# Performance work log

Measured on AMD Instinct MI355X. Metric: run time of the kernel, lower is better.

Reference implementation:

```python
import jax, jax.numpy as jnp
import numpy as np

ALPHA = 2.0
K_HOPS = 3
N_NODES, N_EDGES, IN_DIM = 8192, 131072, 128


def _mlp(coeffs, W0, W1, W2, W3):
    # MLP(n_layers=n_hidden_layers+2=4, relu between, no bias, bn/dropout off in eval)
    h = jax.nn.relu(coeffs @ W0)
    h = jax.nn.relu(h @ W1)
    h = jax.nn.relu(h @ W2)
    return h @ W3  # [N, 1] rotation angles


def _aggregate_k_hop(edge_index, angles):
    # Faithful translation of aggregate_k_hop including its in-place aliasing:
    # enhanced_angles aliases angles, and step_k ACCUMULATES across hops
    # (torch_scatter reduces into the provided out tensor).
    N = angles.shape[0]
    row, col = edge_index[0], edge_index[1]
    f = lambda k: jnp.exp(jnp.asarray(-ALPHA * k, angles.dtype))
    # hop 1: scatter-add over the raw edge list (duplicate edges counted, as in original)
    step = jax.ops.segment_sum(angles[col] * f(1), row, num_segments=N)
    enhanced = angles + step
    # Dense boolean adjacency: composing paths then np.unique(axis=1) is exactly the
    # 'exists a k-step walk' indicator, i.e. boolean adjacency powers.
    adj = jnp.zeros((N, N), jnp.float32).at[row, col].set(1.0)
    P = adj
    for k in range(2, K_HOPS + 1):
        P = ((P @ adj) > 0).astype(jnp.float32)  # unique k-walk pairs
        step = step + f(k) * (P @ enhanced)      # reads angles AFTER previous in-place add
        enhanced = enhanced + step               # step accumulates across hops
    return enhanced


def setup_inputs() -> dict:
    key = jax.random.key(0)
    k0, k1, k2, k3, k4, k5 = jax.random.split(key, 6)
    s = 1.0 / np.sqrt(IN_DIM)
    return {
        "coeffs": jax.random.normal(k0, (N_NODES, IN_DIM), jnp.float32),
        "W0": jax.random.normal(k1, (IN_DIM, IN_DIM), jnp.float32) * s,
        "W1": jax.random.normal(k2, (IN_DIM, IN_DIM), jnp.float32) * s,
        "W2": jax.random.normal(k3, (IN_DIM, IN_DIM), jnp.float32) * s,
        "W3": jax.random.normal(k4, (IN_DIM, 1), jnp.float32) * s,
        "edge_index": jax.random.randint(k5, (2, N_EDGES), 0, N_NODES, dtype=jnp.int32),
    }


def reference(coeffs, W0, W1, W2, W3, edge_index):
    angles = _mlp(coeffs, W0, W1, W2, W3)
    return _aggregate_k_hop(edge_index, angles)  # batch.node_rotation_angles, [N, 1]
```

## Files before the change

kernel.cpp:

```cpp
#include <hip/hip_runtime.h>

constexpr int N    = 8192;
constexpr int NE   = 131072;
constexpr int WPR  = N / 32;
constexpr int MAXD = 64;

#define F1 0.13533528323661270f
#define F2 0.018315638888734179f
#define F3 0.0024787521766663585f

using bf16x8 = __attribute__((ext_vector_type(8))) short;
using f32x4  = __attribute__((ext_vector_type(4))) float;

__device__ __forceinline__ unsigned short f2bf(float f) {
    unsigned int u = __float_as_uint(f);
    u = (u + 0x7FFFu + ((u >> 16) & 1u)) >> 16;
    return (unsigned short)u;
}

__global__ __launch_bounds__(256) void mlp_kernel(
    const float* __restrict__ X,
    const float* __restrict__ W0, const float* __restrict__ W1,
    const float* __restrict__ W2, const float* __restrict__ W3,
    float* __restrict__ angles, float* __restrict__ e1,
    uint4* __restrict__ cntz)
{
    __shared__ unsigned short Xb[16 * 136];
    __shared__ unsigned short Wt[128 * 136];
    __shared__ float part[4][16];

    const int tid  = threadIdx.x;
    const int row0 = blockIdx.x * 16;
    const int nh = tid >> 6, l = tid & 63;
    const int lm = l & 15, lq = l >> 4;

    if (tid < 4) {
        uint4 z; z.x = z.y = z.z = z.w = 0u;
        cntz[blockIdx.x * 4 + tid] = z;
    }

    for (int q = tid; q < 512; q += 256) {
        float4 v = *(const float4*)&X[row0 * 128 + q * 4];
        ushort4 b;
        b.x = f2bf(v.x); b.y = f2bf(v.y); b.z = f2bf(v.z); b.w = f2bf(v.w);
        *(ushort4*)&Xb[(q >> 5) * 136 + (q & 31) * 4] = b;
    }

    for (int layer = 0; layer < 3; ++layer) {
        const float* __restrict__ W = (layer == 0) ? W0 : (layer == 1) ? W1 : W2;
        for (int it = 0; it < 16; ++it) {
            int flat = it * 256 + tid;
            int n  = flat & 127;
            int k0 = (flat >> 7) << 2;
            ushort4 b;
            b.x = f2bf(W[(k0 + 0) * 128 + n]);
            b.y = f2bf(W[(k0 + 1) * 128 + n]);
            b.z = f2bf(W[(k0 + 2) * 128 + n]);
            b.w = f2bf(W[(k0 + 3) * 128 + n]);
            *(ushort4*)&Wt[n * 136 + k0] = b;
        }
        __syncthreads();

        f32x4 acc[2];
#pragma unroll
        for (int t = 0; t < 2; ++t) acc[t] = (f32x4){0.f, 0.f, 0.f, 0.f};

#pragma unroll
        for (int kc = 0; kc < 4; ++kc) {
            bf16x8 a = *(const bf16x8*)&Xb[lm * 136 + kc * 32 + lq * 8];
#pragma unroll
            for (int t = 0; t < 2; ++t) {
                bf16x8 b = *(const bf16x8*)
                    &Wt[(nh * 32 + t * 16 + lm) * 136 + kc * 32 + lq * 8];
                acc[t] = __builtin_amdgcn_mfma_f32_16x16x32_bf16(a, b, acc[t], 0, 0, 0);
            }
        }

#pragma unroll
        for (int t = 0; t < 2; ++t)
#pragma unroll
            for (int r = 0; r < 4; ++r) acc[t][r] = fmaxf(acc[t][r], 0.0f);

        __syncthreads();

        if (layer < 2) {
#pragma unroll
            for (int t = 0; t < 2; ++t)
#pragma unroll
                for (int r = 0; r < 4; ++r)
                    Xb[(lq * 4 + r) * 136 + nh * 32 + t * 16 + lm] =
                        f2bf(acc[t][r]);
        } else {
            float p[4] = {0.f, 0.f, 0.f, 0.f};
#pragma unroll
            for (int t = 0; t < 2; ++t) {
                float w3v = W3[nh * 32 + t * 16 + lm];
#pragma unroll
                for (int r = 0; r < 4; ++r) p[r] += acc[t][r] * w3v;
            }
#pragma unroll
            for (int r = 0; r < 4; ++r) {
                p[r] += __shfl_xor(p[r], 1, 64);
                p[r] += __shfl_xor(p[r], 2, 64);
                p[r] += __shfl_xor(p[r], 4, 64);
                p[r] += __shfl_xor(p[r], 8, 64);
            }
            if (lm == 0)
#pragma unroll
                for (int r = 0; r < 4; ++r)
                    part[nh][lq * 4 + r] = p[r];
            __syncthreads();
            if (tid < 16) {
                float v = part[0][tid] + part[1][tid] + part[2][tid] + part[3][tid];
                angles[row0 + tid] = v;
                e1[row0 + tid] = v;
            }
        }
    }
}

__global__ void edges_kernel(const int* __restrict__ ei,
                             const float* __restrict__ angles,
                             float* __restrict__ e1,
                             int* __restrict__ cnt_g,
                             int* __restrict__ nbr_g)
{
    int e = blockIdx.x * blockDim.x + threadIdx.x;
    if (e < NE) {
        int r = ei[e];
        int c = ei[NE + e];
        int p = atomicAdd(&cnt_g[r], 1);
        if (p < MAXD) nbr_g[r * MAXD + p] = c;
        atomicAdd(&e1[r], F1 * angles[c]);
    }
}

__global__ __launch_bounds__(256) void p2_kernel(
    const int* __restrict__ cnt_g, const int* __restrict__ nbr_g,
    unsigned int* __restrict__ P2,
    const float* __restrict__ angles, const float* __restrict__ e1,
    float* __restrict__ e2, float* __restrict__ es)
{
    __shared__ __align__(16) unsigned int bm[4][WPR];
    __shared__ int nbr[4][MAXD];
    __shared__ int nc[4][MAXD];

    const int wv  = threadIdx.x >> 6;
    const int l   = threadIdx.x & 63;
    const int i   = blockIdx.x * 4 + wv;
    const int qq  = l >> 4;
    const int sub = l & 15;

#pragma unroll
    for (int s = 0; s < 4; ++s) bm[wv][s * 64 + l] = 0u;

    const int n = min(cnt_g[i], MAXD);
    if (l < n) {
        int m = nbr_g[i * MAXD + l];
        nbr[wv][l] = m;
        nc[wv][l]  = min(cnt_g[m], MAXD);
    }
    __syncthreads();

    for (int q0 = 0; q0 < n; q0 += 4) {
        int q = q0 + qq;
        int m = 0, c2 = 0;
        if (q < n) { m = nbr[wv][q]; c2 = nc[wv][q]; }
        for (int s = sub; s < c2; s += 16) {
            int id = nbr_g[m * MAXD + s];
            atomicOr(&bm[wv][id >> 5], 1u << (id & 31));
        }
    }
    __syncthreads();

    uint4 w4 = *(const uint4*)&bm[wv][4 * l];
    *(uint4*)&P2[(size_t)i * WPR + 4 * l] = w4;

    float local = 0.0f;
    unsigned int wrd[4] = {w4.x, w4.y, w4.z, w4.w};
#pragma unroll
    for (int s = 0; s < 4; ++s) {
        unsigned int ww = wrd[s];
        const int base = (4 * l + s) * 32;
        while (ww) {
            int b = __ffs(ww) - 1;
            ww &= ww - 1;
            local += e1[base + b];
        }
    }
#pragma unroll
    for (int m = 1; m < 64; m <<= 1) local += __shfl_xor(local, m, 64);
    if (l == 0) {
        float e1i = e1[i];
        float s1i = e1i - angles[i];
        float s2v = s1i + F2 * local;
        e2[i] = e1i + s2v;
        es[i] = e1i + 2.0f * s2v;
    }
}

__global__ __launch_bounds__(512) void p3_kernel(
    const unsigned int* __restrict__ P2,
    const int* __restrict__ cnt_g, const int* __restrict__ nbr_g,
    const float* __restrict__ e2, const float* __restrict__ es,
    float* __restrict__ out)
{
    __shared__ float e2s[N];
    __shared__ int nbr[8][MAXD];
    __shared__ uint4 bmw[8][64];

    const int tid = threadIdx.x;
    const int wv  = tid >> 6;
    const int l   = tid & 63;
    const int i   = blockIdx.x * 8 + wv;

    for (int q = tid; q < N / 4; q += 512)
        *(float4*)&e2s[q * 4] = *(const float4*)&e2[q * 4];

    const int n = min(cnt_g[i], MAXD);
    if (l < n) nbr[wv][l] = nbr_g[i * MAXD + l];
    __syncthreads();

    uint4 w; w.x = w.y = w.z = w.w = 0u;
    for (int q = 0; q < n; ++q) {
        const uint4* rowp = (const uint4*)(P2 + (size_t)nbr[wv][q] * WPR);
        uint4 r = rowp[l];
        w.x |= r.x; w.y |= r.y; w.z |= r.z; w.w |= r.w;
    }
    bmw[wv][l] = w;
    __syncthreads();

    const unsigned int* bw = (const unsigned int*)&bmw[wv][0];
    float local = 0.0f;
#pragma unroll
    for (int c = 0; c < 32; ++c) {
        unsigned int wd  = bw[c * 8 + (l >> 3)];
        unsigned int nib = wd >> ((l & 7) * 4);
        float4 v = *(const float4*)&e2s[c * 256 + l * 4];
        local += (nib & 1u) ? v.x : 0.0f;
        local += (nib & 2u) ? v.y : 0.0f;
        local += (nib & 4u) ? v.z : 0.0f;
        local += (nib & 8u) ? v.w : 0.0f;
    }
#pragma unroll
    for (int m = 1; m < 64; m <<= 1) local += __shfl_xor(local, m, 64);
    if (l == 0)
        out[i] = es[i] + F3 * local;
}

extern "C" void kernel_launch(void* const* d_in, const int* in_sizes, int n_in,
                              void* d_out, int out_size, void* d_ws, size_t ws_size,
                              hipStream_t stream)
{
    const float* coeffs = (const float*)d_in[0];
    const float* W0     = (const float*)d_in[1];
    const float* W1     = (const float*)d_in[2];
    const float* W2     = (const float*)d_in[3];
    const float* W3     = (const float*)d_in[4];
    const int*   ei     = (const int*)  d_in[5];
    float* out = (float*)d_out;

    char* ws = (char*)d_ws;
    float*          angles = (float*)(ws + 0 * 32768);
    float*          e2     = (float*)(ws + 1 * 32768);
    float*          es     = (float*)(ws + 2 * 32768);
    int*            nbr_g  = (int*)  (ws + (1u  << 20));
    float*          e1     = (float*)(ws + (4u  << 20));
    int*            cnt_g  = (int*)  (ws + (4u  << 20) + 32768);
    unsigned int*   P2     = (unsigned int*)(ws + (5u  << 20));

    mlp_kernel<<<N / 16, 256, 0, stream>>>(coeffs, W0, W1, W2, W3, angles, e1,
                                           (uint4*)cnt_g);

    edges_kernel<<<NE / 256, 256, 0, stream>>>(ei, angles, e1, cnt_g, nbr_g);
    p2_kernel<<<N / 4, 256, 0, stream>>>(cnt_g, nbr_g, P2, angles, e1, e2, es);
    p3_kernel<<<N / 8, 512, 0, stream>>>(P2, cnt_g, nbr_g, e2, es, out);
}
```

Before: 136.9 us.

## Double MLP rows per block, fix p2 LDS bank access, shuffle-based bitmap in p3

The MLP kernel now handles 32 rows per block with a 2x2 wave split (row tile by column half), so each converted weight tile is reused over twice as many rows and half as many blocks are launched. In p2, each lane reads bitmap words strided by 64, which avoids LDS bank conflicts when reading the bitmap. In p3, the shared-memory bitmap staging and its __syncthreads are dropped and words are fetched from registers with __shfl. The trade-off is fewer MLP blocks (256), which may lower occupancy across the GPU's CUs.

```diff
diff --git a/kernel.cpp b/kernel.cpp
--- a/kernel.cpp
+++ b/kernel.cpp
@@ -25,21 +25,22 @@
     float* __restrict__ angles, float* __restrict__ e1,
     uint4* __restrict__ cntz)
 {
-    __shared__ unsigned short Xb[16 * 136];
+    __shared__ unsigned short Xb[32 * 136];
     __shared__ unsigned short Wt[128 * 136];
-    __shared__ float part[4][16];
+    __shared__ float part[2][32];
 
     const int tid  = threadIdx.x;
-    const int row0 = blockIdx.x * 16;
-    const int nh = tid >> 6, l = tid & 63;
+    const int row0 = blockIdx.x * 32;
+    const int w  = tid >> 6, l = tid & 63;
+    const int mt = w & 1, nh = w >> 1;
     const int lm = l & 15, lq = l >> 4;
 
-    if (tid < 4) {
+    if (tid < 8) {
         uint4 z; z.x = z.y = z.z = z.w = 0u;
-        cntz[blockIdx.x * 4 + tid] = z;
-    }
-
-    for (int q = tid; q < 512; q += 256) {
+        cntz[blockIdx.x * 8 + tid] = z;
+    }
+
+    for (int q = tid; q < 32 * 32; q += 256) {
         float4 v = *(const float4*)&X[row0 * 128 + q * 4];
         ushort4 b;
         b.x = f2bf(v.x); b.y = f2bf(v.y); b.z = f2bf(v.z); b.w = f2bf(v.w);
@@ -61,23 +62,23 @@
         }
         __syncthreads();
 
-        f32x4 acc[2];
-#pragma unroll
-        for (int t = 0; t < 2; ++t) acc[t] = (f32x4){0.f, 0.f, 0.f, 0.f};
+        f32x4 acc[4];
+#pragma unroll
+        for (int t = 0; t < 4; ++t) acc[t] = (f32x4){0.f, 0.f, 0.f, 0.f};
 
 #pragma unroll
         for (int kc = 0; kc < 4; ++kc) {
-            bf16x8 a = *(const bf16x8*)&Xb[lm * 136 + kc * 32 + lq * 8];
-#pragma unroll
-            for (int t = 0; t < 2; ++t) {
+            bf16x8 a = *(const bf16x8*)&Xb[(mt * 16 + lm) * 136 + kc * 32 + lq * 8];
+#pragma unroll
+            for (int t = 0; t < 4; ++t) {
                 bf16x8 b = *(const bf16x8*)
-                    &Wt[(nh * 32 + t * 16 + lm) * 136 + kc * 32 + lq * 8];
+                    &Wt[(nh * 64 + t * 16 + lm) * 136 + kc * 32 + lq * 8];
                 acc[t] = __builtin_amdgcn_mfma_f32_16x16x32_bf16(a, b, acc[t], 0, 0, 0);
             }
         }
 
 #pragma unroll
-        for (int t = 0; t < 2; ++t)
+        for (int t = 0; t < 4; ++t)
 #pragma unroll
             for (int r = 0; r < 4; ++r) acc[t][r] = fmaxf(acc[t][r], 0.0f);
 
@@ -85,16 +86,16 @@
 
         if (layer < 2) {
 #pragma unroll
-            for (int t = 0; t < 2; ++t)
+            for (int t = 0; t < 4; ++t)
 #pragma unroll
                 for (int r = 0; r < 4; ++r)
-                    Xb[(lq * 4 + r) * 136 + nh * 32 + t * 16 + lm] =
+                    Xb[(mt * 16 + lq * 4 + r) * 136 + nh * 64 + t * 16 + lm] =
                         f2bf(acc[t][r]);
         } else {
             float p[4] = {0.f, 0.f, 0.f, 0.f};
 #pragma unroll
-            for (int t = 0; t < 2; ++t) {
-                float w3v = W3[nh * 32 + t * 16 + lm];
+            for (int t = 0; t < 4; ++t) {
+                float w3v = W3[nh * 64 + t * 16 + lm];
 #pragma unroll
                 for (int r = 0; r < 4; ++r) p[r] += acc[t][r] * w3v;
             }
@@ -108,10 +109,10 @@
             if (lm == 0)
 #pragma unroll
                 for (int r = 0; r < 4; ++r)
-                    part[nh][lq * 4 + r] = p[r];
+                    part[nh][mt * 16 + lq * 4 + r] = p[r];
             __syncthreads();
-            if (tid < 16) {
-                float v = part[0][tid] + part[1][tid] + part[2][tid] + part[3][tid];
+            if (tid < 32) {
+                float v = part[0][tid] + part[1][tid];
                 angles[row0 + tid] = v;
                 e1[row0 + tid] = v;
             }
@@ -173,15 +174,17 @@
     }
     __syncthreads();
 
-    uint4 w4 = *(const uint4*)&bm[wv][4 * l];
+    unsigned int wrd[4];
+#pragma unroll
+    for (int s = 0; s < 4; ++s) wrd[s] = bm[wv][s * 64 + l];
+    uint4 w4; w4.x = wrd[0]; w4.y = wrd[1]; w4.z = wrd[2]; w4.w = wrd[3];
     *(uint4*)&P2[(size_t)i * WPR + 4 * l] = w4;
 
     float local = 0.0f;
-    unsigned int wrd[4] = {w4.x, w4.y, w4.z, w4.w};
 #pragma unroll
     for (int s = 0; s < 4; ++s) {
         unsigned int ww = wrd[s];
-        const int base = (4 * l + s) * 32;
+        const int base = (s * 64 + l) * 32;
         while (ww) {
             int b = __ffs(ww) - 1;
             ww &= ww - 1;
@@ -207,7 +210,6 @@
 {
     __shared__ float e2s[N];
     __shared__ int nbr[8][MAXD];
-    __shared__ uint4 bmw[8][64];
 
     const int tid = threadIdx.x;
     const int wv  = tid >> 6;
@@ -221,20 +223,17 @@
     if (l < n) nbr[wv][l] = nbr_g[i * MAXD + l];
     __syncthreads();
 
-    uint4 w; w.x = w.y = w.z = w.w = 0u;
+    unsigned int w[4] = {0u, 0u, 0u, 0u};
     for (int q = 0; q < n; ++q) {
         const uint4* rowp = (const uint4*)(P2 + (size_t)nbr[wv][q] * WPR);
         uint4 r = rowp[l];
-        w.x |= r.x; w.y |= r.y; w.z |= r.z; w.w |= r.w;
-    }
-    bmw[wv][l] = w;
-    __syncthreads();
-
-    const unsigned int* bw = (const unsigned int*)&bmw[wv][0];
+        w[0] |= r.x; w[1] |= r.y; w[2] |= r.z; w[3] |= r.w;
+    }
+
     float local = 0.0f;
 #pragma unroll
     for (int c = 0; c < 32; ++c) {
-        unsigned int wd  = bw[c * 8 + (l >> 3)];
+        unsigned int wd  = __shfl(w[c >> 3], ((c & 7) << 3) | (l >> 3), 64);
         unsigned int nib = wd >> ((l & 7) * 4);
         float4 v = *(const float4*)&e2s[c * 256 + l * 4];
         local += (nib & 1u) ? v.x : 0.0f;
@@ -269,7 +268,7 @@
     int*            cnt_g  = (int*)  (ws + (4u  << 20) + 32768);
     unsigned int*   P2     = (unsigned int*)(ws + (5u  << 20));
 
-    mlp_kernel<<<N / 16, 256, 0, stream>>>(coeffs, W0, W1, W2, W3, angles, e1,
+    mlp_kernel<<<N / 32, 256, 0, stream>>>(coeffs, W0, W1, W2, W3, angles, e1,
                                            (uint4*)cnt_g);
 
     edges_kernel<<<NE / 256, 256, 0, stream>>>(ei, angles, e1, cnt_g, nbr_g);
```

Result: faster. 116.9 us (-14.6%).
